# Kernel tuning notes

Measured on AMD Instinct MI355X. Metric: run time of the kernel, lower is better.

Reference implementation:

```python
import jax, jax.numpy as jnp
import numpy as np

B, N, D, L = 16, 2048, 128, 3  # batch, n_sensors, node_hidden_dim, conv layers
LN_EPS = 1e-5


def setup_inputs() -> dict:
    key = jax.random.key(0)
    k_x, k_a, k_w = jax.random.split(key, 3)
    X = jax.random.normal(k_x, (B, N, D), dtype=jnp.float32)
    adj_mat = jax.random.uniform(k_a, (B, N, N), dtype=jnp.float32)
    # Xavier-uniform-ish GCN weights (lin has no bias in GCNConv; bias added post-aggregation)
    limit = np.sqrt(6.0 / (D + D))
    Ws = jax.random.uniform(k_w, (L, D, D), dtype=jnp.float32, minval=-limit, maxval=limit)
    bs = jnp.zeros((L, D), dtype=jnp.float32)
    gammas = jnp.ones((L, D), dtype=jnp.float32)
    betas = jnp.zeros((L, D), dtype=jnp.float32)
    return {"X": X, "adj_mat": adj_mat, "Ws": Ws, "bs": bs, "gammas": gammas, "betas": betas}


def _layer_norm(z, gamma, beta):
    mu = jnp.mean(z, axis=-1, keepdims=True)
    var = jnp.mean(jnp.square(z - mu), axis=-1, keepdims=True)
    return (z - mu) * jax.lax.rsqrt(var + LN_EPS) * gamma + beta


def reference(X, adj_mat, Ws, bs, gammas, betas):
    # GCNConv(add_self_loops=False, normalize=False) with edge weights from
    # dense_to_sparse(adj) is exactly: out[j] = sum_i adj[i,j] * (h @ W)[i] + b,
    # i.e. adj^T @ (h @ W) + b, batched over B.
    h = X
    for i in range(L):
        res = h
        hw = jnp.einsum('bnd,de->bne', h, Ws[i])           # linear (no bias)
        agg = jnp.einsum('bij,bie->bje', adj_mat, hw)       # adj^T aggregation
        conv = agg + bs[i]
        h = jax.nn.relu(_layer_norm(conv + res, gammas[i], betas[i]))
    return h
```

## Files before the change

### kernel.cpp

```cpp
#include <hip/hip_runtime.h>

#define BB 16
#define NN 2048
#define DD 128
#define KS 4
#define KC (NN / KS)

typedef __attribute__((ext_vector_type(8))) __bf16 bf16x8;
typedef __attribute__((ext_vector_type(4))) float f32x4;
typedef __attribute__((ext_vector_type(4))) unsigned int u32x4;
typedef __attribute__((address_space(3))) unsigned int lds_u32;
typedef __attribute__((address_space(1))) const unsigned int glob_u32;

static __device__ __forceinline__ unsigned short f2b(float f) {
  union { float f; unsigned int u; } c; c.f = f;
  unsigned int u = c.u;
  unsigned int r = (u + 0x7FFFu + ((u >> 16) & 1u)) >> 16;
  return (unsigned short)r;
}
static __device__ __forceinline__ float b2f(unsigned short u) {
  union { unsigned int u; float f; } c; c.u = ((unsigned int)u) << 16;
  return c.f;
}

__global__ void k_wt(const float* __restrict__ W, unsigned short* __restrict__ WT) {
  __shared__ float t[64][65];
  int l = blockIdx.z, d0 = blockIdx.x * 64, e0 = blockIdx.y * 64;
  int tid = threadIdx.x;
  const float* src = W + (size_t)l * DD * DD;
  for (int p = 0; p < 16; ++p) {
    int idx = p * 256 + tid;
    int d = idx >> 6, e = idx & 63;
    t[e][d] = src[(size_t)(d0 + d) * DD + (e0 + e)];
  }
  __syncthreads();
  unsigned short* dst = WT + (size_t)l * DD * DD;
  for (int p = 0; p < 4; ++p) {
    int idx = p * 256 + tid;
    int e = idx >> 4, d4 = (idx & 15) * 4;
    ushort4 r;
    r.x = f2b(t[e][d4 + 0]); r.y = f2b(t[e][d4 + 1]);
    r.z = f2b(t[e][d4 + 2]); r.w = f2b(t[e][d4 + 3]);
    *(ushort4*)(dst + (size_t)(e0 + e) * DD + (d0 + d4)) = r;
  }
}

__global__ __launch_bounds__(256) void k_pre(const float* __restrict__ adj,
                                             unsigned short* __restrict__ adjT,
                                             const float* __restrict__ X,
                                             const unsigned short* __restrict__ WT,
                                             unsigned short* __restrict__ hwT) {
  int b = blockIdx.y, x = blockIdx.x, tid = threadIdx.x;
  if (x < 1024) {
    __shared__ float t[64][65];
    int j0 = (x >> 5) * 64, i0 = (x & 31) * 64;
    const float* src = adj + (size_t)b * NN * NN;
    for (int p = 0; p < 16; ++p) {
      int idx = p * 256 + tid;
      int i = idx >> 6, j = idx & 63;
      t[j][i] = src[(size_t)(i0 + i) * NN + (j0 + j)];
    }
    __syncthreads();
    unsigned short* dst = adjT + (size_t)b * NN * NN;
    for (int p = 0; p < 4; ++p) {
      int idx = p * 256 + tid;
      int j = idx >> 4, i4 = (idx & 15) * 4;
      ushort4 r;
      r.x = f2b(t[j][i4 + 0]); r.y = f2b(t[j][i4 + 1]);
      r.z = f2b(t[j][i4 + 2]); r.w = f2b(t[j][i4 + 3]);
      *(ushort4*)(dst + (size_t)(j0 + j) * NN + (i0 + i4)) = r;
    }
  } else {
    int i0 = (x - 1024) * 64;
    int lane = tid & 63, w = tid >> 6;
    int q = lane >> 4, m = lane & 15;
    f32x4 acc[8];
#pragma unroll
    for (int t = 0; t < 8; ++t)
#pragma unroll
      for (int r = 0; r < 4; ++r) acc[t][r] = 0.f;
    int irow = i0 + w * 16 + m;
    const float* hrow = X + ((size_t)b * NN + irow) * DD;
#pragma unroll
    for (int kk = 0; kk < 4; ++kk) {
      int d0 = kk * 32 + q * 8;
      float4 h0 = *(const float4*)(hrow + d0);
      float4 h1 = *(const float4*)(hrow + d0 + 4);
      union { bf16x8 v; unsigned short s[8]; } ub;
      ub.s[0] = f2b(h0.x); ub.s[1] = f2b(h0.y); ub.s[2] = f2b(h0.z); ub.s[3] = f2b(h0.w);
      ub.s[4] = f2b(h1.x); ub.s[5] = f2b(h1.y); ub.s[6] = f2b(h1.z); ub.s[7] = f2b(h1.w);
#pragma unroll
      for (int mt = 0; mt < 8; ++mt) {
        bf16x8 af = *(const bf16x8*)(WT + (mt * 16 + m) * 128 + d0);
        acc[mt] = __builtin_amdgcn_mfma_f32_16x16x32_bf16(af, ub.v, acc[mt], 0, 0, 0);
      }
    }
    unsigned short* dst = hwT + (size_t)b * DD * NN;
#pragma unroll
    for (int mt = 0; mt < 8; ++mt)
#pragma unroll
      for (int r = 0; r < 4; ++r)
        dst[(size_t)(mt * 16 + q * 4 + r) * NN + irow] = f2b(acc[mt][r]);
  }
}

__global__ __launch_bounds__(256) void k_gemm2(const unsigned short* __restrict__ adjT,
                                               const unsigned short* __restrict__ hwT,
                                               unsigned short* __restrict__ pacc) {
  __shared__ __align__(16) unsigned short sAB[16384];
  unsigned short* sA = sAB;
  unsigned short* sH = sAB + 8192;
  int tid = threadIdx.x;
  int lane = tid & 63, w = tid >> 6;
  int q = lane >> 4, m = lane & 15;
  int wj = w & 1, we = w >> 1;
  int b = blockIdx.y, j0 = blockIdx.x * 128, ks = blockIdx.z;
  const unsigned short* At = adjT + (size_t)b * NN * NN;
  const unsigned short* Ht = hwT + (size_t)b * DD * NN;

  const unsigned short* aSrc[4];
  const unsigned short* hSrc[4];
#pragma unroll
  for (int it = 0; it < 4; ++it) {
    int p = (w * 4 + it) * 64 + lane;
    int r = p >> 3, cg = (p & 7) ^ (r & 7);
    aSrc[it] = At + (size_t)(j0 + r) * NN + ks * KC + cg * 8;
    hSrc[it] = Ht + (size_t)r * NN + ks * KC + cg * 8;
  }

  f32x4 acc[4][4];
#pragma unroll
  for (int i = 0; i < 4; ++i)
#pragma unroll
    for (int j = 0; j < 4; ++j)
#pragma unroll
      for (int r = 0; r < 4; ++r) acc[i][j][r] = 0.f;

  for (int k0 = 0; k0 < KC; k0 += 64) {
    __syncthreads();
#pragma unroll
    for (int it = 0; it < 4; ++it) {
      __builtin_amdgcn_global_load_lds((glob_u32*)aSrc[it],
                                       (lds_u32*)(sA + (w * 4 + it) * 512), 16, 0, 0);
      __builtin_amdgcn_global_load_lds((glob_u32*)hSrc[it],
                                       (lds_u32*)(sH + (w * 4 + it) * 512), 16, 0, 0);
      aSrc[it] += 64; hSrc[it] += 64;
    }
    __syncthreads();
#pragma unroll
    for (int kk = 0; kk < 2; ++kk) {
      bf16x8 af[4], bf[4];
#pragma unroll
      for (int mt = 0; mt < 4; ++mt) {
        int r = wj * 64 + mt * 16 + m;
        int c = (kk * 4 + q) ^ (r & 7);
        af[mt] = *(const bf16x8*)(sA + r * 64 + c * 8);
      }
#pragma unroll
      for (int nt = 0; nt < 4; ++nt) {
        int r = we * 64 + nt * 16 + m;
        int c = (kk * 4 + q) ^ (r & 7);
        bf[nt] = *(const bf16x8*)(sH + r * 64 + c * 8);
      }
#pragma unroll
      for (int mt = 0; mt < 4; ++mt)
#pragma unroll
        for (int nt = 0; nt < 4; ++nt)
          acc[mt][nt] = __builtin_amdgcn_mfma_f32_16x16x32_bf16(af[mt], bf[nt], acc[mt][nt], 0, 0, 0);
    }
  }
  __syncthreads();
#pragma unroll
  for (int mt = 0; mt < 4; ++mt)
#pragma unroll
    for (int nt = 0; nt < 4; ++nt)
#pragma unroll
      for (int r = 0; r < 4; ++r) {
        int row = wj * 64 + mt * 16 + q * 4 + r;
        int col = we * 64 + nt * 16 + m;
        sAB[row * 128 + col] = f2b(acc[mt][nt][r]);
      }
  __syncthreads();
  unsigned short* P = pacc + ((size_t)ks * BB + b) * (size_t)NN * DD + (size_t)j0 * DD;
#pragma unroll
  for (int p = 0; p < 8; ++p) {
    int idx = p * 256 + tid;
    int row = idx >> 4, c8 = (idx & 15) * 8;
    *(u32x4*)(P + (size_t)row * DD + c8) = *(const u32x4*)(sAB + row * 128 + c8);
  }
}

__global__ __launch_bounds__(256) void k_rg1(const unsigned short* __restrict__ pacc,
                                             const float* __restrict__ res,
                                             const float* __restrict__ bias,
                                             const float* __restrict__ gamma,
                                             const float* __restrict__ beta,
                                             const unsigned short* __restrict__ WTn,
                                             float* __restrict__ outf,
                                             unsigned short* __restrict__ hwT,
                                             int doW) {
  __shared__ float z[64 * 132];
  __shared__ float smu[64], srs[64];
  __shared__ unsigned short sW[128 * 132];
  int tid = threadIdx.x;
  int lane = tid & 63, w = tid >> 6;
  int q = lane >> 4, m = lane & 15;
  int b = blockIdx.y, j0 = blockIdx.x * 64;
  if (doW) {
#pragma unroll
    for (int p = 0; p < 8; ++p) {
      int idx = p * 256 + tid;
      int e = idx >> 4, d8 = (idx & 15) * 8;
      *(u32x4*)(sW + e * 132 + d8) = *(const u32x4*)(WTn + e * 128 + d8);
    }
  }
  size_t base = ((size_t)b * NN + j0) * DD;
  const size_t kstride = (size_t)BB * NN * DD;
  const unsigned short* P = pacc + base;
#pragma unroll
  for (int p = 0; p < 4; ++p) {
    int idx = p * 256 + tid;
    int j = idx >> 4, c8 = (idx & 15) * 8;
    size_t off = (size_t)j * DD + c8;
    float v[8];
    const float4* r4 = (const float4*)(res + base + off);
    float4 r0 = r4[0], r1 = r4[1];
    const float4* bi4 = (const float4*)(bias + c8);
    float4 b0 = bi4[0], b1 = bi4[1];
    v[0] = r0.x + b0.x; v[1] = r0.y + b0.y; v[2] = r0.z + b0.z; v[3] = r0.w + b0.w;
    v[4] = r1.x + b1.x; v[5] = r1.y + b1.y; v[6] = r1.z + b1.z; v[7] = r1.w + b1.w;
#pragma unroll
    for (int s = 0; s < KS; ++s) {
      union { u32x4 u; unsigned short h[8]; } up;
      up.u = *(const u32x4*)(P + s * kstride + off);
#pragma unroll
      for (int t = 0; t < 8; ++t) v[t] += b2f(up.h[t]);
    }
#pragma unroll
    for (int t = 0; t < 8; ++t) z[j * 132 + c8 + t] = v[t];
  }
  __syncthreads();
  {
    int j = tid >> 2, s = tid & 3;
    float sum = 0.f, sq = 0.f;
#pragma unroll
    for (int k = 0; k < 32; ++k) {
      float v = z[j * 132 + s + 4 * k];
      sum += v; sq += v * v;
    }
    sum += __shfl_xor(sum, 1); sq += __shfl_xor(sq, 1);
    sum += __shfl_xor(sum, 2); sq += __shfl_xor(sq, 2);
    if (s == 0) {
      float mu = sum * (1.f / 128.f);
      float var = sq * (1.f / 128.f) - mu * mu;
      smu[j] = mu;
      srs[j] = rsqrtf(var + 1e-5f);
    }
  }
  __syncthreads();
  {
    int e = tid & 127;
    float g = gamma[e], bt = beta[e];
#pragma unroll
    for (int p = 0; p < 32; ++p) {
      int idx = p * 256 + tid;
      int j = idx >> 7;
      float v = (z[j * 132 + e] - smu[j]) * srs[j] * g + bt;
      v = fmaxf(v, 0.f);
      outf[base + idx] = v;
      z[j * 132 + e] = v;
    }
  }
  if (!doW) return;
  __syncthreads();
  f32x4 acc[8];
#pragma unroll
  for (int t = 0; t < 8; ++t)
#pragma unroll
    for (int r = 0; r < 4; ++r) acc[t][r] = 0.f;
  int irow = j0 + w * 16 + m;
  const float* hrow = &z[(w * 16 + m) * 132];
#pragma unroll
  for (int kk = 0; kk < 4; ++kk) {
    int d0 = kk * 32 + q * 8;
    float4 h0 = *(const float4*)(hrow + d0);
    float4 h1 = *(const float4*)(hrow + d0 + 4);
    union { bf16x8 v; unsigned short s[8]; } ub;
    ub.s[0] = f2b(h0.x); ub.s[1] = f2b(h0.y); ub.s[2] = f2b(h0.z); ub.s[3] = f2b(h0.w);
    ub.s[4] = f2b(h1.x); ub.s[5] = f2b(h1.y); ub.s[6] = f2b(h1.z); ub.s[7] = f2b(h1.w);
#pragma unroll
    for (int mt = 0; mt < 8; ++mt) {
      bf16x8 af = *(const bf16x8*)(sW + (mt * 16 + m) * 132 + d0);
      acc[mt] = __builtin_amdgcn_mfma_f32_16x16x32_bf16(af, ub.v, acc[mt], 0, 0, 0);
    }
  }
  unsigned short* dst = hwT + (size_t)b * DD * NN;
#pragma unroll
  for (int mt = 0; mt < 8; ++mt)
#pragma unroll
    for (int r = 0; r < 4; ++r)
      dst[(size_t)(mt * 16 + q * 4 + r) * NN + irow] = f2b(acc[mt][r]);
}

extern "C" void kernel_launch(void* const* d_in, const int* in_sizes, int n_in,
                              void* d_out, int out_size, void* d_ws, size_t ws_size,
                              hipStream_t stream) {
  const float* X   = (const float*)d_in[0];
  const float* adj = (const float*)d_in[1];
  const float* Ws  = (const float*)d_in[2];
  const float* bs  = (const float*)d_in[3];
  const float* gms = (const float*)d_in[4];
  const float* bts = (const float*)d_in[5];
  float* out = (float*)d_out;

  unsigned short* adjT = (unsigned short*)d_ws;
  unsigned short* hwT  = adjT + (size_t)BB * NN * NN;
  unsigned short* pacc = hwT + (size_t)BB * DD * NN;
  unsigned short* WT   = pacc + (size_t)KS * BB * NN * DD;

  k_wt<<<dim3(2, 2, 3), 256, 0, stream>>>(Ws, WT);
  k_pre<<<dim3(1056, BB), 256, 0, stream>>>(adj, adjT, X, WT, hwT);
  for (int l = 0; l < 3; ++l) {
    k_gemm2<<<dim3(NN / 128, BB, KS), 256, 0, stream>>>(adjT, hwT, pacc);
    const float* res = (l == 0) ? X : (const float*)out;
    const unsigned short* WTn = WT + (size_t)((l < 2) ? (l + 1) : 0) * DD * DD;
    k_rg1<<<dim3(NN / 64, BB), 256, 0, stream>>>(pacc, res, bs + l * DD,
                                                 gms + l * DD, bts + l * DD,
                                                 WTn, out, hwT, (l < 2) ? 1 : 0);
  }
}
```

Baseline: 243.7 us.

## Fuse aggregation GEMM with LayerNorm epilogue, drop split-K, double-buffer LDS

The split-K aggregation GEMM and the separate reduce/LayerNorm/next-linear kernel are merged into one per-layer kernel. Each block now covers 64 nodes over the full K range. It double-buffers adjacency and hw tiles in LDS with async global-to-LDS loads, so the next tile loads while the current one computes. The fp32 accumulator goes straight into the LayerNorm epilogue, which removes the bf16 partial-sum buffer round trip and one launch per layer. hw is ping-ponged between two buffers so blocks cannot read a tile another block has already overwritten. The cost is 512 blocks instead of 1024, each with a longer serial K loop, and W is now read from global rather than LDS.

```diff
diff --git a/kernel.cpp b/kernel.cpp
--- a/kernel.cpp
+++ b/kernel.cpp
@@ -3,8 +3,6 @@
 #define BB 16
 #define NN 2048
 #define DD 128
-#define KS 4
-#define KC (NN / KS)
 
 typedef __attribute__((ext_vector_type(8))) __bf16 bf16x8;
 typedef __attribute__((ext_vector_type(4))) float f32x4;
@@ -17,10 +15,6 @@
   unsigned int u = c.u;
   unsigned int r = (u + 0x7FFFu + ((u >> 16) & 1u)) >> 16;
   return (unsigned short)r;
-}
-static __device__ __forceinline__ float b2f(unsigned short u) {
-  union { unsigned int u; float f; } c; c.u = ((unsigned int)u) << 16;
-  return c.f;
 }
 
 __global__ void k_wt(const float* __restrict__ W, unsigned short* __restrict__ WT) {
@@ -104,55 +98,76 @@
   }
 }
 
-__global__ __launch_bounds__(256) void k_gemm2(const unsigned short* __restrict__ adjT,
-                                               const unsigned short* __restrict__ hwT,
-                                               unsigned short* __restrict__ pacc) {
-  __shared__ __align__(16) unsigned short sAB[16384];
-  unsigned short* sA = sAB;
-  unsigned short* sH = sAB + 8192;
+__global__ __launch_bounds__(256) void k_layer(const unsigned short* __restrict__ adjT,
+                                               const unsigned short* __restrict__ hwT_in,
+                                               const float* __restrict__ res,
+                                               const float* __restrict__ bias,
+                                               const float* __restrict__ gamma,
+                                               const float* __restrict__ beta,
+                                               const unsigned short* __restrict__ WTn,
+                                               float* __restrict__ outf,
+                                               unsigned short* __restrict__ hwT_out,
+                                               int doW) {
+  __shared__ __align__(16) unsigned char smem[49152];
   int tid = threadIdx.x;
   int lane = tid & 63, w = tid >> 6;
   int q = lane >> 4, m = lane & 15;
   int wj = w & 1, we = w >> 1;
-  int b = blockIdx.y, j0 = blockIdx.x * 128, ks = blockIdx.z;
+  int b = blockIdx.y, j0 = blockIdx.x * 64;
+
   const unsigned short* At = adjT + (size_t)b * NN * NN;
-  const unsigned short* Ht = hwT + (size_t)b * DD * NN;
-
-  const unsigned short* aSrc[4];
+  const unsigned short* Ht = hwT_in + (size_t)b * DD * NN;
+
+  const unsigned short* aSrc[2];
   const unsigned short* hSrc[4];
+#pragma unroll
+  for (int it = 0; it < 2; ++it) {
+    int p = (w * 2 + it) * 64 + lane;
+    int r = p >> 3, cg = (p & 7) ^ (r & 7);
+    aSrc[it] = At + (size_t)(j0 + r) * NN + cg * 8;
+  }
 #pragma unroll
   for (int it = 0; it < 4; ++it) {
     int p = (w * 4 + it) * 64 + lane;
     int r = p >> 3, cg = (p & 7) ^ (r & 7);
-    aSrc[it] = At + (size_t)(j0 + r) * NN + ks * KC + cg * 8;
-    hSrc[it] = Ht + (size_t)r * NN + ks * KC + cg * 8;
-  }
-
-  f32x4 acc[4][4];
-#pragma unroll
-  for (int i = 0; i < 4; ++i)
-#pragma unroll
-    for (int j = 0; j < 4; ++j)
-#pragma unroll
-      for (int r = 0; r < 4; ++r) acc[i][j][r] = 0.f;
-
-  for (int k0 = 0; k0 < KC; k0 += 64) {
-    __syncthreads();
-#pragma unroll
-    for (int it = 0; it < 4; ++it) {
-      __builtin_amdgcn_global_load_lds((glob_u32*)aSrc[it],
-                                       (lds_u32*)(sA + (w * 4 + it) * 512), 16, 0, 0);
-      __builtin_amdgcn_global_load_lds((glob_u32*)hSrc[it],
-                                       (lds_u32*)(sH + (w * 4 + it) * 512), 16, 0, 0);
-      aSrc[it] += 64; hSrc[it] += 64;
-    }
-    __syncthreads();
+    hSrc[it] = Ht + (size_t)r * NN + cg * 8;
+  }
+
+#define STAGE_K(bufbase)                                                              \
+  do {                                                                                \
+    _Pragma("unroll") for (int it = 0; it < 2; ++it) {                                \
+      __builtin_amdgcn_global_load_lds((glob_u32*)aSrc[it],                           \
+          (lds_u32*)((bufbase) + (w * 2 + it) * 1024 + lane * 16), 16, 0, 0);         \
+      aSrc[it] += 64;                                                                 \
+    }                                                                                 \
+    _Pragma("unroll") for (int it = 0; it < 4; ++it) {                                \
+      __builtin_amdgcn_global_load_lds((glob_u32*)hSrc[it],                           \
+          (lds_u32*)((bufbase) + 8192 + (w * 4 + it) * 1024 + lane * 16), 16, 0, 0);  \
+      hSrc[it] += 64;                                                                 \
+    }                                                                                 \
+  } while (0)
+
+  f32x4 acc[2][4];
+#pragma unroll
+  for (int mt = 0; mt < 2; ++mt)
+#pragma unroll
+    for (int nt = 0; nt < 4; ++nt)
+#pragma unroll
+      for (int r = 0; r < 4; ++r) acc[mt][nt][r] = 0.f;
+
+  STAGE_K(smem);
+  __syncthreads();
+  int cur = 0;
+  for (int t = 0; t < 32; ++t) {
+    if (t < 31) STAGE_K(smem + (cur ^ 1) * 24576);
+    const unsigned short* sA = (const unsigned short*)(smem + cur * 24576);
+    const unsigned short* sH = sA + 4096;
 #pragma unroll
     for (int kk = 0; kk < 2; ++kk) {
-      bf16x8 af[4], bf[4];
-#pragma unroll
-      for (int mt = 0; mt < 4; ++mt) {
-        int r = wj * 64 + mt * 16 + m;
+      bf16x8 af[2], bv[4];
+#pragma unroll
+      for (int mt = 0; mt < 2; ++mt) {
+        int r = wj * 32 + mt * 16 + m;
         int c = (kk * 4 + q) ^ (r & 7);
         af[mt] = *(const bf16x8*)(sA + r * 64 + c * 8);
       }
@@ -160,86 +175,50 @@
       for (int nt = 0; nt < 4; ++nt) {
         int r = we * 64 + nt * 16 + m;
         int c = (kk * 4 + q) ^ (r & 7);
-        bf[nt] = *(const bf16x8*)(sH + r * 64 + c * 8);
+        bv[nt] = *(const bf16x8*)(sH + r * 64 + c * 8);
       }
 #pragma unroll
-      for (int mt = 0; mt < 4; ++mt)
+      for (int mt = 0; mt < 2; ++mt)
 #pragma unroll
         for (int nt = 0; nt < 4; ++nt)
-          acc[mt][nt] = __builtin_amdgcn_mfma_f32_16x16x32_bf16(af[mt], bf[nt], acc[mt][nt], 0, 0, 0);
-    }
-  }
-  __syncthreads();
-#pragma unroll
-  for (int mt = 0; mt < 4; ++mt)
+          acc[mt][nt] = __builtin_amdgcn_mfma_f32_16x16x32_bf16(af[mt], bv[nt], acc[mt][nt], 0, 0, 0);
+    }
+    __syncthreads();
+    cur ^= 1;
+  }
+#undef STAGE_K
+
+  float* z = (float*)smem;
+  float* smu = (float*)(smem + 33792);
+  float* srs = (float*)(smem + 34048);
+
+#pragma unroll
+  for (int mt = 0; mt < 2; ++mt)
 #pragma unroll
     for (int nt = 0; nt < 4; ++nt)
 #pragma unroll
       for (int r = 0; r < 4; ++r) {
-        int row = wj * 64 + mt * 16 + q * 4 + r;
+        int row = wj * 32 + mt * 16 + q * 4 + r;
         int col = we * 64 + nt * 16 + m;
-        sAB[row * 128 + col] = f2b(acc[mt][nt][r]);
+        z[row * 132 + col] = acc[mt][nt][r];
       }
   __syncthreads();
-  unsigned short* P = pacc + ((size_t)ks * BB + b) * (size_t)NN * DD + (size_t)j0 * DD;
-#pragma unroll
-  for (int p = 0; p < 8; ++p) {
-    int idx = p * 256 + tid;
-    int row = idx >> 4, c8 = (idx & 15) * 8;
-    *(u32x4*)(P + (size_t)row * DD + c8) = *(const u32x4*)(sAB + row * 128 + c8);
-  }
-}
-
-__global__ __launch_bounds__(256) void k_rg1(const unsigned short* __restrict__ pacc,
-                                             const float* __restrict__ res,
-                                             const float* __restrict__ bias,
-                                             const float* __restrict__ gamma,
-                                             const float* __restrict__ beta,
-                                             const unsigned short* __restrict__ WTn,
-                                             float* __restrict__ outf,
-                                             unsigned short* __restrict__ hwT,
-                                             int doW) {
-  __shared__ float z[64 * 132];
-  __shared__ float smu[64], srs[64];
-  __shared__ unsigned short sW[128 * 132];
-  int tid = threadIdx.x;
-  int lane = tid & 63, w = tid >> 6;
-  int q = lane >> 4, m = lane & 15;
-  int b = blockIdx.y, j0 = blockIdx.x * 64;
-  if (doW) {
-#pragma unroll
-    for (int p = 0; p < 8; ++p) {
-      int idx = p * 256 + tid;
-      int e = idx >> 4, d8 = (idx & 15) * 8;
-      *(u32x4*)(sW + e * 132 + d8) = *(const u32x4*)(WTn + e * 128 + d8);
-    }
-  }
+
   size_t base = ((size_t)b * NN + j0) * DD;
-  const size_t kstride = (size_t)BB * NN * DD;
-  const unsigned short* P = pacc + base;
 #pragma unroll
   for (int p = 0; p < 4; ++p) {
     int idx = p * 256 + tid;
     int j = idx >> 4, c8 = (idx & 15) * 8;
-    size_t off = (size_t)j * DD + c8;
-    float v[8];
-    const float4* r4 = (const float4*)(res + base + off);
+    const float4* r4 = (const float4*)(res + base + (size_t)j * DD + c8);
     float4 r0 = r4[0], r1 = r4[1];
     const float4* bi4 = (const float4*)(bias + c8);
     float4 b0 = bi4[0], b1 = bi4[1];
-    v[0] = r0.x + b0.x; v[1] = r0.y + b0.y; v[2] = r0.z + b0.z; v[3] = r0.w + b0.w;
-    v[4] = r1.x + b1.x; v[5] = r1.y + b1.y; v[6] = r1.z + b1.z; v[7] = r1.w + b1.w;
-#pragma unroll
-    for (int s = 0; s < KS; ++s) {
-      union { u32x4 u; unsigned short h[8]; } up;
-      up.u = *(const u32x4*)(P + s * kstride + off);
-#pragma unroll
-      for (int t = 0; t < 8; ++t) v[t] += b2f(up.h[t]);
-    }
-#pragma unroll
-    for (int t = 0; t < 8; ++t) z[j * 132 + c8 + t] = v[t];
-  }
-  __syncthreads();
+    float* zp = z + j * 132 + c8;
+    zp[0] += r0.x + b0.x; zp[1] += r0.y + b0.y; zp[2] += r0.z + b0.z; zp[3] += r0.w + b0.w;
+    zp[4] += r1.x + b1.x; zp[5] += r1.y + b1.y; zp[6] += r1.z + b1.z; zp[7] += r1.w + b1.w;
+  }
+  __syncthreads();
+
   {
     int j = tid >> 2, s = tid & 3;
     float sum = 0.f, sq = 0.f;
@@ -258,6 +237,7 @@
     }
   }
   __syncthreads();
+
   {
     int e = tid & 127;
     float g = gamma[e], bt = beta[e];
@@ -273,13 +253,13 @@
   }
   if (!doW) return;
   __syncthreads();
-  f32x4 acc[8];
+
+  f32x4 a2[8];
 #pragma unroll
   for (int t = 0; t < 8; ++t)
 #pragma unroll
-    for (int r = 0; r < 4; ++r) acc[t][r] = 0.f;
-  int irow = j0 + w * 16 + m;
-  const float* hrow = &z[(w * 16 + m) * 132];
+    for (int r = 0; r < 4; ++r) a2[t][r] = 0.f;
+  const float* hrow = z + (w * 16 + m) * 132;
 #pragma unroll
   for (int kk = 0; kk < 4; ++kk) {
     int d0 = kk * 32 + q * 8;
@@ -290,16 +270,17 @@
     ub.s[4] = f2b(h1.x); ub.s[5] = f2b(h1.y); ub.s[6] = f2b(h1.z); ub.s[7] = f2b(h1.w);
 #pragma unroll
     for (int mt = 0; mt < 8; ++mt) {
-      bf16x8 af = *(const bf16x8*)(sW + (mt * 16 + m) * 132 + d0);
-      acc[mt] = __builtin_amdgcn_mfma_f32_16x16x32_bf16(af, ub.v, acc[mt], 0, 0, 0);
-    }
-  }
-  unsigned short* dst = hwT + (size_t)b * DD * NN;
+      bf16x8 af = *(const bf16x8*)(WTn + (mt * 16 + m) * 128 + d0);
+      a2[mt] = __builtin_amdgcn_mfma_f32_16x16x32_bf16(af, ub.v, a2[mt], 0, 0, 0);
+    }
+  }
+  unsigned short* dst = hwT_out + (size_t)b * DD * NN;
+  int irow = j0 + w * 16 + m;
 #pragma unroll
   for (int mt = 0; mt < 8; ++mt)
 #pragma unroll
     for (int r = 0; r < 4; ++r)
-      dst[(size_t)(mt * 16 + q * 4 + r) * NN + irow] = f2b(acc[mt][r]);
+      dst[(size_t)(mt * 16 + q * 4 + r) * NN + irow] = f2b(a2[mt][r]);
 }
 
 extern "C" void kernel_launch(void* const* d_in, const int* in_sizes, int n_in,
@@ -314,18 +295,20 @@
   float* out = (float*)d_out;
 
   unsigned short* adjT = (unsigned short*)d_ws;
-  unsigned short* hwT  = adjT + (size_t)BB * NN * NN;
-  unsigned short* pacc = hwT + (size_t)BB * DD * NN;
-  unsigned short* WT   = pacc + (size_t)KS * BB * NN * DD;
+  unsigned short* hwTA = adjT + (size_t)BB * NN * NN;
+  unsigned short* hwTB = hwTA + (size_t)BB * DD * NN;
+  unsigned short* WT   = hwTB + (size_t)BB * DD * NN;
 
   k_wt<<<dim3(2, 2, 3), 256, 0, stream>>>(Ws, WT);
-  k_pre<<<dim3(1056, BB), 256, 0, stream>>>(adj, adjT, X, WT, hwT);
+  k_pre<<<dim3(1056, BB), 256, 0, stream>>>(adj, adjT, X, WT, hwTA);
+  unsigned short* hin = hwTA;
+  unsigned short* hout = hwTB;
   for (int l = 0; l < 3; ++l) {
-    k_gemm2<<<dim3(NN / 128, BB, KS), 256, 0, stream>>>(adjT, hwT, pacc);
     const float* res = (l == 0) ? X : (const float*)out;
     const unsigned short* WTn = WT + (size_t)((l < 2) ? (l + 1) : 0) * DD * DD;
-    k_rg1<<<dim3(NN / 64, BB), 256, 0, stream>>>(pacc, res, bs + l * DD,
-                                                 gms + l * DD, bts + l * DD,
-                                                 WTn, out, hwT, (l < 2) ? 1 : 0);
-  }
-}
+    k_layer<<<dim3(NN / 64, BB), 256, 0, stream>>>(adjT, hin, res, bs + l * DD,
+                                                   gms + l * DD, bts + l * DD,
+                                                   WTn, out, hout, (l < 2) ? 1 : 0);
+    unsigned short* tmp = hin; hin = hout; hout = tmp;
+  }
+}
```

After: 218.0 us. -10.6%, faster.
